# Kernel optimization log

Hardware: AMD Instinct MI355X
Metric: run time of the kernel (lower is better)

Reference implementation:

```python
import jax, jax.numpy as jnp
import numpy as np
from jax import lax

K = 3
PAD = 1
STRIDE = 1
DIL = 1
BN_EPS = 1e-5


def bilinear_gather(x, py, px):
    """Zero-padded bilinear sampling. x:[B,C,Hin,Win]; py,px:[B,T,H,W] -> [B,C,T,H,W]."""
    B, C, Hin, Win = x.shape
    xf = x.reshape(B, C, Hin * Win)
    y0 = jnp.floor(py)
    x0 = jnp.floor(px)
    wy1 = py - y0
    wx1 = px - x0
    wy0 = 1.0 - wy1
    wx0 = 1.0 - wx1

    def corner(yc, xc, w):
        valid = (yc >= 0) & (yc <= Hin - 1) & (xc >= 0) & (xc <= Win - 1)
        yi = jnp.clip(yc, 0, Hin - 1).astype(jnp.int32)
        xi = jnp.clip(xc, 0, Win - 1).astype(jnp.int32)
        idx = (yi * Win + xi).reshape(B, -1)  # [B, T*H*W]
        vals = jax.vmap(lambda xb, ib: xb[:, ib])(xf, idx)  # [B, C, T*H*W]
        vals = vals.reshape(B, C, *py.shape[1:])
        return vals * (w * valid.astype(x.dtype))[:, None]

    return (corner(y0, x0, wy0 * wx0) + corner(y0, x0 + 1.0, wy0 * wx1)
            + corner(y0 + 1.0, x0, wy1 * wx0) + corner(y0 + 1.0, x0 + 1.0, wy1 * wx1))


def setup_inputs() -> dict:
    key = jax.random.key(0)
    ks = jax.random.split(key, 6)
    B, C, H, W, O = 8, 128, 80, 80, 128
    x = jax.random.normal(ks[0], (B, C, H, W), dtype=jnp.float32)
    # offset/mask conv (zero-init in the module; small random here so sampling is exercised)
    w_off = jax.random.normal(ks[1], (3 * K * K, C, K, K), dtype=jnp.float32) * 0.05
    b_off = jax.random.normal(ks[2], (3 * K * K,), dtype=jnp.float32) * 0.01
    # main DCN weight: uniform(-std, std), std = 1/sqrt(C*K*K)
    std = 1.0 / float(np.sqrt(C * K * K))
    w_dcn = jax.random.uniform(ks[3], (O, C, K, K), dtype=jnp.float32, minval=-std, maxval=std)
    b_dcn = jax.random.normal(ks[4], (O,), dtype=jnp.float32) * 0.01
    gamma = jnp.ones((O,), dtype=jnp.float32)
    beta = jnp.zeros((O,), dtype=jnp.float32)
    return {"x": x, "w_dcn": w_dcn, "b_dcn": b_dcn, "w_off": w_off, "b_off": b_off,
            "gamma": gamma, "beta": beta}


def reference(x, w_dcn, b_dcn, w_off, b_off, gamma, beta):
    B, C, H, W = x.shape
    O = w_dcn.shape[0]
    # offset/mask conv (k=3, s=1, p=1) -> [B, 27, H, W]
    om = lax.conv_general_dilated(x, w_off, (STRIDE, STRIDE), [(PAD, PAD), (PAD, PAD)],
                                  dimension_numbers=("NCHW", "OIHW", "NCHW"))
    om = om + b_off[None, :, None, None]
    o1, o2, m = jnp.split(om, 3, axis=1)  # each [B, 9, H, W]
    mask = jax.nn.sigmoid(m)
    # torch: offset = cat(o1, o2); torchvision reads channel 2t as dy_t, 2t+1 as dx_t
    off = jnp.concatenate([o1, o2], axis=1).reshape(B, K * K, 2, H, W)
    dy, dx = off[:, :, 0], off[:, :, 1]  # [B, 9, H, W]
    ky, kx = jnp.meshgrid(jnp.arange(K), jnp.arange(K), indexing="ij")
    ky = ky.reshape(-1)
    kx = kx.reshape(-1)  # [9]
    base_y = (jnp.arange(H)[None, :, None] * STRIDE - PAD + ky[:, None, None] * DIL).astype(x.dtype)  # [9,H,1]
    base_x = (jnp.arange(W)[None, None, :] * STRIDE - PAD + kx[:, None, None] * DIL).astype(x.dtype)  # [9,1,W]
    py = dy + base_y[None]  # [B, 9, H, W]
    px = dx + base_x[None]
    sampled = bilinear_gather(x, py, px)  # [B, C, 9, H, W]
    sampled = sampled * mask[:, None]  # modulated (dg=1 broadcasts over C)
    wk = w_dcn.reshape(O, C, K * K)
    out = jnp.einsum("bckhw,ock->bohw", sampled, wk) + b_dcn[None, :, None, None]
    # BatchNorm (training-mode batch stats, biased variance) + SiLU
    mu = out.mean(axis=(0, 2, 3), keepdims=True)
    var = out.var(axis=(0, 2, 3), keepdims=True)
    y = (out - mu) * lax.rsqrt(var + BN_EPS) * gamma[None, :, None, None] + beta[None, :, None, None]
    return y * jax.nn.sigmoid(y)
```

## Files before the change

### kernel.cpp

```cpp
#include <hip/hip_runtime.h>
#include <hip/hip_bf16.h>
#include <hip/hip_fp16.h>

constexpr int B = 8, C = 128, H = 80, W = 80, O = 128;
constexpr int HW = H * W;
constexpr int NPIX = B * HW;
constexpr int KC = C * 9;
constexpr int DPX = 64;
constexpr int NBLK = NPIX / DPX;

typedef _Float16 h8 __attribute__((ext_vector_type(8)));
typedef _Float16 h2 __attribute__((ext_vector_type(2)));
typedef float f32x4 __attribute__((ext_vector_type(4)));

__device__ inline h8 as_h8(uint4 v) { h8 r; __builtin_memcpy(&r, &v, 16); return r; }
__device__ inline h2 u2h(uint u) { h2 r; __builtin_memcpy(&r, &u, 4); return r; }
__device__ inline uint h2u(h2 h) { uint r; __builtin_memcpy(&r, &h, 4); return r; }
__device__ inline uint pkh(float a, float b) {
  h2 h = { (_Float16)a, (_Float16)b };
  return h2u(h);
}
__device__ inline int swz16(int row, int byte) {
  return (row * 256 + (byte ^ ((row & 7) << 4))) >> 1;
}

__global__ __launch_bounds__(256) void k_xt(const float* __restrict__ x,
                                            _Float16* __restrict__ xt) {
  __shared__ uint tile32[64 * 64];
  const int t = threadIdx.x;
  const int p0 = blockIdx.x * 64;
  const int b = p0 / HW, hw0 = p0 - b * HW;
  const int w = t >> 6, l = t & 63;
#pragma unroll
  for (int j = 0; j < 16; ++j) {
    int c0 = (j * 4 + w) * 2;
    float f0 = x[((size_t)(b * C + c0)) * HW + hw0 + l];
    float f1 = x[((size_t)(b * C + c0 + 1)) * HW + hw0 + l];
    int byte = l * 256 + ((c0 * 2) ^ ((l & 7) << 4));
    tile32[byte >> 2] = pkh(f0, f1);
  }
  __syncthreads();
  _Float16* dst = xt + (size_t)(b * HW + hw0) * C;
#pragma unroll
  for (int it = 0; it < 4; ++it) {
    int g = w * 4096 + it * 1024 + l * 16;
    int row = g >> 8, inner = g & 255;
    uint4 v = *(const uint4*)((const char*)tile32 + row * 256 + (inner ^ ((row & 7) << 4)));
    *(uint4*)(dst + (g >> 1)) = v;
  }
}

__global__ __launch_bounds__(256) void k_wt2(const float* __restrict__ w_dcn,
                                             const float* __restrict__ w_off,
                                             _Float16* __restrict__ wt,
                                             _Float16* __restrict__ wof,
                                             _Float16* __restrict__ zrow) {
  int i = blockIdx.x * 256 + threadIdx.x;
  if (i < O * KC) {
    int c = i & 127, k = (i >> 7) % 9, o = i / KC;
    wt[i] = (_Float16)w_dcn[(size_t)o * KC + c * 9 + k];
  }
  if (i < 32 * KC) {
    int c = i & 127, k = (i >> 7) % 9, o = i / KC;
    wof[i] = (o < 27) ? (_Float16)w_off[((size_t)o * C + c) * 9 + k] : (_Float16)0.f;
  }
  if (i < 128) zrow[i] = (_Float16)0.f;
}

__global__ __launch_bounds__(256, 6) void k_offc4(
    const _Float16* __restrict__ xt, const _Float16* __restrict__ wof,
    const _Float16* __restrict__ zrow, const float* __restrict__ b_off,
    float* __restrict__ om) {
  const int t = threadIdx.x;
  const int bid = (blockIdx.x & 7) * 200 + (blockIdx.x >> 3);
  const int b = bid / 200, hw0 = (bid - b * 200) * 32;
  const int lane = t & 63, wv = t >> 6, rl = lane & 15, gh = lane >> 4;
  const int mi = wv & 1, nt = wv >> 1;
  const int px = hw0 + nt * 16 + rl;
  const int hp = px / W, wp = px - hp * W;
  const _Float16* xb = xt + (size_t)b * HW * C;
  f32x4 acc = {0.f, 0.f, 0.f, 0.f};
#pragma unroll
  for (int k = 0; k < 9; ++k) {
    int ky = k / 3, kx = k - ky * 3;
    int y = hp + ky - 1, xx = wp + kx - 1;
    bool ok = ((unsigned)y < (unsigned)H) && ((unsigned)xx < (unsigned)W);
    const _Float16* rowp = ok ? (xb + (size_t)(y * W + xx) * C) : zrow;
    const _Float16* aP = wof + (size_t)(mi * 16 + rl) * KC + k * 128 + gh * 8;
#pragma unroll
    for (int kk = 0; kk < 4; ++kk) {
      h8 av = *(const h8*)(aP + kk * 32);
      h8 bv = *(const h8*)(rowp + kk * 32 + gh * 8);
      acc = __builtin_amdgcn_mfma_f32_16x16x32_f16(av, bv, acc, 0, 0, 0);
    }
  }
  float* ob = om + (size_t)b * 27 * HW + hw0 + nt * 16 + rl;
#pragma unroll
  for (int r = 0; r < 4; ++r) {
    int oc = mi * 16 + gh * 4 + r;
    if (oc < 27) ob[(size_t)oc * HW] = acc[r] + b_off[oc];
  }
}

__global__ __launch_bounds__(256, 3) void k_dcn4(
    const _Float16* __restrict__ xt, const float* __restrict__ om,
    const _Float16* __restrict__ wt, float* __restrict__ outr,
    float* __restrict__ part2) {
  __shared__ float s_w[DPX][9][4];
  __shared__ int s_i[DPX][9][4];
  __shared__ __align__(16) ushort s_buf[2][DPX * 128];
  const int t = threadIdx.x;
  const int bid = (blockIdx.x & 7) * 100 + (blockIdx.x >> 3);
  const int b = bid / 100, hw0 = (bid - b * 100) * DPX;

  for (int idx = t; idx < DPX * 9; idx += 256) {
    int px = idx / 9, k = idx - (idx / 9) * 9;
    int hw = hw0 + px, h = hw / W, w = hw - (hw / W) * W;
    int ky = k / 3, kx = k - ky * 3;
    const float* omp = om + (size_t)b * 27 * HW + hw;
    float dy = omp[(size_t)(2 * k) * HW];
    float dx = omp[(size_t)(2 * k + 1) * HW];
    float mk = 1.0f / (1.0f + __expf(-omp[(size_t)(18 + k) * HW]));
    float py = dy + (float)(h - 1 + ky);
    float pxf = dx + (float)(w - 1 + kx);
    float y0f = floorf(py), x0f = floorf(pxf);
    float wy1 = py - y0f, wx1 = pxf - x0f;
    float wy0 = 1.0f - wy1, wx0 = 1.0f - wx1;
    int y0 = (int)y0f, x0 = (int)x0f;
    int y1 = y0 + 1, x1 = x0 + 1;
    bool vy0 = (y0 >= 0) && (y0 < H);
    bool vy1 = (y1 >= 0) && (y1 < H);
    bool vx0 = (x0 >= 0) && (x0 < W);
    bool vx1 = (x1 >= 0) && (x1 < W);
    int cy0 = min(max(y0, 0), H - 1), cy1 = min(max(y1, 0), H - 1);
    int cx0 = min(max(x0, 0), W - 1), cx1 = min(max(x1, 0), W - 1);
    s_w[px][k][0] = (vy0 && vx0) ? wy0 * wx0 * mk : 0.0f;
    s_w[px][k][1] = (vy0 && vx1) ? wy0 * wx1 * mk : 0.0f;
    s_w[px][k][2] = (vy1 && vx0) ? wy1 * wx0 * mk : 0.0f;
    s_w[px][k][3] = (vy1 && vx1) ? wy1 * wx1 * mk : 0.0f;
    s_i[px][k][0] = cy0 * W + cx0;
    s_i[px][k][1] = cy0 * W + cx1;
    s_i[px][k][2] = cy1 * W + cx0;
    s_i[px][k][3] = cy1 * W + cx1;
  }
  __syncthreads();

  const int sp = t >> 2, sq = t & 3;
  const _Float16* xbq = xt + (size_t)b * HW * C + sq * 32;
  const int lane = t & 63, wv = t >> 6, rl = lane & 15, gh = lane >> 4;
  const _Float16* wbase = wt + (size_t)(wv * 32 + rl) * KC + gh * 8;

  uint4 gA0, gA1, gA2, gA3, gB0, gB1, gB2, gB3;
  uint4 gC0, gC1, gC2, gC3, gD0, gD1, gD2, gD3;
  uint4 wA0, wA1, wA2, wA3, wB0, wB1, wB2, wB3;
  float cw0, cw1, cw2, cw3;

#define GL4(o0, o1, o2, o3, P)                                            \
  asm volatile("global_load_dwordx4 %0, %4, off\n\t"                      \
               "global_load_dwordx4 %1, %4, off offset:16\n\t"            \
               "global_load_dwordx4 %2, %4, off offset:32\n\t"            \
               "global_load_dwordx4 %3, %4, off offset:48"                \
               : "=&v"(o0), "=&v"(o1), "=&v"(o2), "=&v"(o3) : "v"(P))
#define WL4(o0, o1, o2, o3, P)                                            \
  asm volatile("global_load_dwordx4 %0, %4, off\n\t"                      \
               "global_load_dwordx4 %1, %4, off offset:64\n\t"            \
               "global_load_dwordx4 %2, %4, off offset:128\n\t"           \
               "global_load_dwordx4 %3, %4, off offset:192"               \
               : "=&v"(o0), "=&v"(o1), "=&v"(o2), "=&v"(o3) : "v"(P))

  auto GLOAD = [&](int k) {
    int4 ii = *(const int4*)&s_i[sp][k][0];
    float4 wf = *(const float4*)&s_w[sp][k][0];
    cw0 = wf.x; cw1 = wf.y; cw2 = wf.z; cw3 = wf.w;
    GL4(gA0, gA1, gA2, gA3, xbq + (size_t)ii.x * C);
    GL4(gB0, gB1, gB2, gB3, xbq + (size_t)ii.y * C);
    GL4(gC0, gC1, gC2, gC3, xbq + (size_t)ii.z * C);
    GL4(gD0, gD1, gD2, gD3, xbq + (size_t)ii.w * C);
  };
  auto WLOAD = [&](int k) {
    const _Float16* a0 = wbase + k * 128;
    WL4(wA0, wA1, wA2, wA3, a0);
    WL4(wB0, wB1, wB2, wB3, a0 + 16 * KC);
  };

  auto SWRITE = [&](ushort* buf) {
    uint qa[16] = {gA0.x, gA0.y, gA0.z, gA0.w, gA1.x, gA1.y, gA1.z, gA1.w,
                   gA2.x, gA2.y, gA2.z, gA2.w, gA3.x, gA3.y, gA3.z, gA3.w};
    uint qb[16] = {gB0.x, gB0.y, gB0.z, gB0.w, gB1.x, gB1.y, gB1.z, gB1.w,
                   gB2.x, gB2.y, gB2.z, gB2.w, gB3.x, gB3.y, gB3.z, gB3.w};
    uint qc[16] = {gC0.x, gC0.y, gC0.z, gC0.w, gC1.x, gC1.y, gC1.z, gC1.w,
                   gC2.x, gC2.y, gC2.z, gC2.w, gC3.x, gC3.y, gC3.z, gC3.w};
    uint qd[16] = {gD0.x, gD0.y, gD0.z, gD0.w, gD1.x, gD1.y, gD1.z, gD1.w,
                   gD2.x, gD2.y, gD2.z, gD2.w, gD3.x, gD3.y, gD3.z, gD3.w};
    h2 W0 = {(_Float16)cw0, (_Float16)cw0};
    h2 W1 = {(_Float16)cw1, (_Float16)cw1};
    h2 W2 = {(_Float16)cw2, (_Float16)cw2};
    h2 W3 = {(_Float16)cw3, (_Float16)cw3};
    uint r[16];
#pragma unroll
    for (int d = 0; d < 16; ++d) {
      h2 o = u2h(qa[d]) * W0 + u2h(qb[d]) * W1 + u2h(qc[d]) * W2 + u2h(qd[d]) * W3;
      r[d] = h2u(o);
    }
#pragma unroll
    for (int e = 0; e < 4; ++e)
      *(uint4*)(buf + swz16(sp, sq * 64 + e * 16)) =
          make_uint4(r[4 * e], r[4 * e + 1], r[4 * e + 2], r[4 * e + 3]);
  };

  f32x4 acc[2][4];
#pragma unroll
  for (int m = 0; m < 2; ++m)
#pragma unroll
    for (int nt = 0; nt < 4; ++nt) acc[m][nt] = {0.f, 0.f, 0.f, 0.f};

  auto COMP = [&](const ushort* buf) {
    h8 av0, av1, bv;
#define KSTEP(WA, WB, KB)                                                  \
  av0 = as_h8(WA); av1 = as_h8(WB);                                        \
  _Pragma("unroll")                                                        \
  for (int nt = 0; nt < 4; ++nt) {                                         \
    bv = *(const h8*)(buf + swz16(nt * 16 + rl, KB + gh * 16));            \
    acc[0][nt] = __builtin_amdgcn_mfma_f32_16x16x32_f16(av0, bv, acc[0][nt], 0, 0, 0); \
    acc[1][nt] = __builtin_amdgcn_mfma_f32_16x16x32_f16(av1, bv, acc[1][nt], 0, 0, 0); \
  }
    KSTEP(wA0, wB0, 0)
    KSTEP(wA1, wB1, 64)
    KSTEP(wA2, wB2, 128)
    KSTEP(wA3, wB3, 192)
#undef KSTEP
  };

  GLOAD(0); WLOAD(0);
  asm volatile("s_waitcnt vmcnt(8)" ::: "memory");
  __builtin_amdgcn_sched_barrier(0);
  SWRITE(s_buf[0]);
  __syncthreads();

  for (int k = 0; k < 9; ++k) {
    if (k < 8) GLOAD(k + 1);
    if (k < 8) asm volatile("s_waitcnt vmcnt(16)" ::: "memory");
    else       asm volatile("s_waitcnt vmcnt(0)" ::: "memory");
    __builtin_amdgcn_sched_barrier(0);
    COMP(s_buf[k & 1]);
    if (k < 8) {
      WLOAD(k + 1);
      asm volatile("s_waitcnt vmcnt(8)" ::: "memory");
      __builtin_amdgcn_sched_barrier(0);
      SWRITE(s_buf[(k + 1) & 1]);
      __syncthreads();
    }
  }
#undef GL4
#undef WL4

  float* outb = outr + (size_t)b * O * HW + hw0 + rl;
  const int nb = blockIdx.x;
#pragma unroll
  for (int mi = 0; mi < 2; ++mi)
#pragma unroll
    for (int r = 0; r < 4; ++r) {
      int o = wv * 32 + mi * 16 + gh * 4 + r;
      float s = 0.f, s2 = 0.f;
#pragma unroll
      for (int nt = 0; nt < 4; ++nt) {
        float v = acc[mi][nt][r];
        outb[(size_t)o * HW + nt * 16] = v;
        s += v;
        s2 = fmaf(v, v, s2);
      }
#pragma unroll
      for (int m = 1; m < 16; m <<= 1) {
        s += __shfl_xor(s, m);
        s2 += __shfl_xor(s2, m);
      }
      if (rl == 0) {
        part2[(size_t)(2 * o) * NBLK + nb] = s;
        part2[(size_t)(2 * o + 1) * NBLK + nb] = s2;
      }
    }
}

__global__ __launch_bounds__(256) void k_bnred(const float* __restrict__ part2,
                                               float* __restrict__ stats) {
  const int j = blockIdx.x;
  float s = 0.f;
  for (int i = threadIdx.x; i < NBLK; i += 256) s += part2[(size_t)j * NBLK + i];
#pragma unroll
  for (int off = 32; off > 0; off >>= 1) s += __shfl_down(s, off);
  __shared__ float rs[4];
  int wid = threadIdx.x >> 6, lane = threadIdx.x & 63;
  if (lane == 0) rs[wid] = s;
  __syncthreads();
  if (threadIdx.x == 0) stats[j] = rs[0] + rs[1] + rs[2] + rs[3];
}

__global__ __launch_bounds__(256) void k_bnapply2(
    float* __restrict__ outr, const float* __restrict__ stats,
    const float* __restrict__ gamma, const float* __restrict__ beta) {
  const int n4 = B * O * HW / 4;
  for (int i = blockIdx.x * blockDim.x + threadIdx.x; i < n4;
       i += gridDim.x * blockDim.x) {
    int o = (i / (HW / 4)) % O;
    float S = stats[2 * o], S2 = stats[2 * o + 1];
    const float inv = 1.0f / (float)(B * HW);
    float mu = S * inv;
    float rstd = rsqrtf(fmaf(S2, inv, -mu * mu) + 1e-5f);
    float a = rstd * gamma[o];
    float bb = fmaf(-mu, a, beta[o]);
    float4 v = ((const float4*)outr)[i];
    float y0 = fmaf(v.x, a, bb);
    float y1 = fmaf(v.y, a, bb);
    float y2 = fmaf(v.z, a, bb);
    float y3 = fmaf(v.w, a, bb);
    v.x = y0 / (1.0f + __expf(-y0));
    v.y = y1 / (1.0f + __expf(-y1));
    v.z = y2 / (1.0f + __expf(-y2));
    v.w = y3 / (1.0f + __expf(-y3));
    ((float4*)outr)[i] = v;
  }
}

extern "C" void kernel_launch(void* const* d_in, const int* in_sizes, int n_in,
                              void* d_out, int out_size, void* d_ws, size_t ws_size,
                              hipStream_t stream) {
  const float* x = (const float*)d_in[0];
  const float* w_dcn = (const float*)d_in[1];
  const float* w_off = (const float*)d_in[3];
  const float* b_off = (const float*)d_in[4];
  const float* gamma = (const float*)d_in[5];
  const float* beta = (const float*)d_in[6];
  float* out = (float*)d_out;
  float* om = (float*)d_ws;
  _Float16* xt = (_Float16*)(om + (size_t)B * 27 * HW);
  _Float16* wt = xt + (size_t)B * HW * C;
  _Float16* wof = wt + (size_t)O * KC;
  float* part2 = (float*)(wof + (size_t)32 * KC);
  float* stats = part2 + (size_t)256 * NBLK;
  _Float16* zrow = (_Float16*)(stats + 256);

  k_xt<<<NPIX / 64, 256, 0, stream>>>(x, xt);
  k_wt2<<<(O * KC + 255) / 256, 256, 0, stream>>>(w_dcn, w_off, wt, wof, zrow);
  k_offc4<<<NPIX / 32, 256, 0, stream>>>(xt, wof, zrow, b_off, om);
  k_dcn4<<<NPIX / DPX, 256, 0, stream>>>(xt, om, wt, out, part2);
  k_bnred<<<256, 256, 0, stream>>>(part2, stats);
  k_bnapply2<<<2048, 256, 0, stream>>>(out, stats, gamma, beta);
}
```

Baseline: 230.5 us.

## Gather bilinear samples directly into MFMA registers, dropping LDS staging

The deformable-conv main kernel no longer stages interpolated samples through a double-buffered LDS tile with block barriers. Each wave now gathers and interpolates its own 16 pixels straight into MFMA B-operand registers and covers all 128 output channels per wave, loading weights directly from global memory (L2-cached). BN partial sums are combined across waves in shared memory before one store per block. This removes LDS writes, reads and syncs, but every wave re-reads the full weight slice, uses more accumulator registers (occupancy hint lowered from 3 to 2), and the weight loads are no longer prefetched.

```diff
diff --git a/kernel.cpp b/kernel.cpp
--- a/kernel.cpp
+++ b/kernel.cpp
@@ -19,9 +19,6 @@
 __device__ inline uint pkh(float a, float b) {
   h2 h = { (_Float16)a, (_Float16)b };
   return h2u(h);
-}
-__device__ inline int swz16(int row, int byte) {
-  return (row * 256 + (byte ^ ((row & 7) << 4))) >> 1;
 }
 
 __global__ __launch_bounds__(256) void k_xt(const float* __restrict__ x,
@@ -102,13 +99,13 @@
   }
 }
 
-__global__ __launch_bounds__(256, 3) void k_dcn4(
+__global__ __launch_bounds__(256, 2) void k_dcn5(
     const _Float16* __restrict__ xt, const float* __restrict__ om,
     const _Float16* __restrict__ wt, float* __restrict__ outr,
     float* __restrict__ part2) {
   __shared__ float s_w[DPX][9][4];
   __shared__ int s_i[DPX][9][4];
-  __shared__ __align__(16) ushort s_buf[2][DPX * 128];
+  __shared__ float s_red[2][128][4];
   const int t = threadIdx.x;
   const int bid = (blockIdx.x & 7) * 100 + (blockIdx.x >> 3);
   const int b = bid / 100, hw0 = (bid - b * 100) * DPX;
@@ -145,140 +142,108 @@
   }
   __syncthreads();
 
-  const int sp = t >> 2, sq = t & 3;
-  const _Float16* xbq = xt + (size_t)b * HW * C + sq * 32;
   const int lane = t & 63, wv = t >> 6, rl = lane & 15, gh = lane >> 4;
-  const _Float16* wbase = wt + (size_t)(wv * 32 + rl) * KC + gh * 8;
-
-  uint4 gA0, gA1, gA2, gA3, gB0, gB1, gB2, gB3;
-  uint4 gC0, gC1, gC2, gC3, gD0, gD1, gD2, gD3;
-  uint4 wA0, wA1, wA2, wA3, wB0, wB1, wB2, wB3;
-  float cw0, cw1, cw2, cw3;
-
-#define GL4(o0, o1, o2, o3, P)                                            \
-  asm volatile("global_load_dwordx4 %0, %4, off\n\t"                      \
-               "global_load_dwordx4 %1, %4, off offset:16\n\t"            \
-               "global_load_dwordx4 %2, %4, off offset:32\n\t"            \
-               "global_load_dwordx4 %3, %4, off offset:48"                \
+  const int mypx = wv * 16 + rl;
+  const _Float16* xb = xt + (size_t)b * HW * C + gh * 8;
+
+  uint4 pa0, pa1, pa2, pa3, pb0, pb1, pb2, pb3;
+  uint4 pc0, pc1, pc2, pc3, pd0, pd1, pd2, pd3;
+  float4 wf;
+
+#define GLD4(o0, o1, o2, o3, P)                                           \
+  asm volatile("global_load_dwordx4 %0, %4, off\n\t"                     \
+               "global_load_dwordx4 %1, %4, off offset:64\n\t"           \
+               "global_load_dwordx4 %2, %4, off offset:128\n\t"          \
+               "global_load_dwordx4 %3, %4, off offset:192"              \
                : "=&v"(o0), "=&v"(o1), "=&v"(o2), "=&v"(o3) : "v"(P))
-#define WL4(o0, o1, o2, o3, P)                                            \
-  asm volatile("global_load_dwordx4 %0, %4, off\n\t"                      \
-               "global_load_dwordx4 %1, %4, off offset:64\n\t"            \
-               "global_load_dwordx4 %2, %4, off offset:128\n\t"           \
-               "global_load_dwordx4 %3, %4, off offset:192"               \
-               : "=&v"(o0), "=&v"(o1), "=&v"(o2), "=&v"(o3) : "v"(P))
-
-  auto GLOAD = [&](int k) {
-    int4 ii = *(const int4*)&s_i[sp][k][0];
-    float4 wf = *(const float4*)&s_w[sp][k][0];
-    cw0 = wf.x; cw1 = wf.y; cw2 = wf.z; cw3 = wf.w;
-    GL4(gA0, gA1, gA2, gA3, xbq + (size_t)ii.x * C);
-    GL4(gB0, gB1, gB2, gB3, xbq + (size_t)ii.y * C);
-    GL4(gC0, gC1, gC2, gC3, xbq + (size_t)ii.z * C);
-    GL4(gD0, gD1, gD2, gD3, xbq + (size_t)ii.w * C);
+
+  auto ISSUE = [&](int k) {
+    int4 ii = *(const int4*)&s_i[mypx][k][0];
+    wf = *(const float4*)&s_w[mypx][k][0];
+    GLD4(pa0, pa1, pa2, pa3, xb + (size_t)ii.x * C);
+    GLD4(pb0, pb1, pb2, pb3, xb + (size_t)ii.y * C);
+    GLD4(pc0, pc1, pc2, pc3, xb + (size_t)ii.z * C);
+    GLD4(pd0, pd1, pd2, pd3, xb + (size_t)ii.w * C);
   };
-  auto WLOAD = [&](int k) {
-    const _Float16* a0 = wbase + k * 128;
-    WL4(wA0, wA1, wA2, wA3, a0);
-    WL4(wB0, wB1, wB2, wB3, a0 + 16 * KC);
-  };
-
-  auto SWRITE = [&](ushort* buf) {
-    uint qa[16] = {gA0.x, gA0.y, gA0.z, gA0.w, gA1.x, gA1.y, gA1.z, gA1.w,
-                   gA2.x, gA2.y, gA2.z, gA2.w, gA3.x, gA3.y, gA3.z, gA3.w};
-    uint qb[16] = {gB0.x, gB0.y, gB0.z, gB0.w, gB1.x, gB1.y, gB1.z, gB1.w,
-                   gB2.x, gB2.y, gB2.z, gB2.w, gB3.x, gB3.y, gB3.z, gB3.w};
-    uint qc[16] = {gC0.x, gC0.y, gC0.z, gC0.w, gC1.x, gC1.y, gC1.z, gC1.w,
-                   gC2.x, gC2.y, gC2.z, gC2.w, gC3.x, gC3.y, gC3.z, gC3.w};
-    uint qd[16] = {gD0.x, gD0.y, gD0.z, gD0.w, gD1.x, gD1.y, gD1.z, gD1.w,
-                   gD2.x, gD2.y, gD2.z, gD2.w, gD3.x, gD3.y, gD3.z, gD3.w};
-    h2 W0 = {(_Float16)cw0, (_Float16)cw0};
-    h2 W1 = {(_Float16)cw1, (_Float16)cw1};
-    h2 W2 = {(_Float16)cw2, (_Float16)cw2};
-    h2 W3 = {(_Float16)cw3, (_Float16)cw3};
-    uint r[16];
-#pragma unroll
-    for (int d = 0; d < 16; ++d) {
-      h2 o = u2h(qa[d]) * W0 + u2h(qb[d]) * W1 + u2h(qc[d]) * W2 + u2h(qd[d]) * W3;
-      r[d] = h2u(o);
+
+  f32x4 acc[8];
+#pragma unroll
+  for (int m = 0; m < 8; ++m) acc[m] = {0.f, 0.f, 0.f, 0.f};
+
+  ISSUE(0);
+  __builtin_amdgcn_sched_barrier(0);
+
+  for (int k = 0; k < 9; ++k) {
+    h2 W0 = {(_Float16)wf.x, (_Float16)wf.x};
+    h2 W1 = {(_Float16)wf.y, (_Float16)wf.y};
+    h2 W2 = {(_Float16)wf.z, (_Float16)wf.z};
+    h2 W3 = {(_Float16)wf.w, (_Float16)wf.w};
+    uint4 bf0, bf1, bf2, bf3;
+
+    asm volatile("s_waitcnt vmcnt(8)" ::: "memory");
+    __builtin_amdgcn_sched_barrier(0);
+#define I1(DST, A, Bq)                                                    \
+  DST.x = h2u(u2h(A.x) * W0 + u2h(Bq.x) * W1);                            \
+  DST.y = h2u(u2h(A.y) * W0 + u2h(Bq.y) * W1);                            \
+  DST.z = h2u(u2h(A.z) * W0 + u2h(Bq.z) * W1);                            \
+  DST.w = h2u(u2h(A.w) * W0 + u2h(Bq.w) * W1);
+    I1(bf0, pa0, pb0) I1(bf1, pa1, pb1) I1(bf2, pa2, pb2) I1(bf3, pa3, pb3)
+#undef I1
+    asm volatile("s_waitcnt vmcnt(0)" ::: "memory");
+    __builtin_amdgcn_sched_barrier(0);
+#define I2(DST, Cq, D)                                                    \
+  DST.x = h2u(u2h(DST.x) + u2h(Cq.x) * W2 + u2h(D.x) * W3);               \
+  DST.y = h2u(u2h(DST.y) + u2h(Cq.y) * W2 + u2h(D.y) * W3);               \
+  DST.z = h2u(u2h(DST.z) + u2h(Cq.z) * W2 + u2h(D.z) * W3);               \
+  DST.w = h2u(u2h(DST.w) + u2h(Cq.w) * W2 + u2h(D.w) * W3);
+    I2(bf0, pc0, pd0) I2(bf1, pc1, pd1) I2(bf2, pc2, pd2) I2(bf3, pc3, pd3)
+#undef I2
+    __builtin_amdgcn_sched_barrier(0);
+
+    h8 b0 = as_h8(bf0), b1 = as_h8(bf1), b2 = as_h8(bf2), b3 = as_h8(bf3);
+    __builtin_amdgcn_s_setprio(1);
+#pragma unroll
+    for (int m = 0; m < 8; ++m) {
+      const _Float16* ap = wt + (size_t)(m * 16 + rl) * KC + k * 128 + gh * 8;
+      acc[m] = __builtin_amdgcn_mfma_f32_16x16x32_f16(*(const h8*)(ap), b0, acc[m], 0, 0, 0);
+      acc[m] = __builtin_amdgcn_mfma_f32_16x16x32_f16(*(const h8*)(ap + 32), b1, acc[m], 0, 0, 0);
+      acc[m] = __builtin_amdgcn_mfma_f32_16x16x32_f16(*(const h8*)(ap + 64), b2, acc[m], 0, 0, 0);
+      acc[m] = __builtin_amdgcn_mfma_f32_16x16x32_f16(*(const h8*)(ap + 96), b3, acc[m], 0, 0, 0);
     }
-#pragma unroll
-    for (int e = 0; e < 4; ++e)
-      *(uint4*)(buf + swz16(sp, sq * 64 + e * 16)) =
-          make_uint4(r[4 * e], r[4 * e + 1], r[4 * e + 2], r[4 * e + 3]);
-  };
-
-  f32x4 acc[2][4];
-#pragma unroll
-  for (int m = 0; m < 2; ++m)
-#pragma unroll
-    for (int nt = 0; nt < 4; ++nt) acc[m][nt] = {0.f, 0.f, 0.f, 0.f};
-
-  auto COMP = [&](const ushort* buf) {
-    h8 av0, av1, bv;
-#define KSTEP(WA, WB, KB)                                                  \
-  av0 = as_h8(WA); av1 = as_h8(WB);                                        \
-  _Pragma("unroll")                                                        \
-  for (int nt = 0; nt < 4; ++nt) {                                         \
-    bv = *(const h8*)(buf + swz16(nt * 16 + rl, KB + gh * 16));            \
-    acc[0][nt] = __builtin_amdgcn_mfma_f32_16x16x32_f16(av0, bv, acc[0][nt], 0, 0, 0); \
-    acc[1][nt] = __builtin_amdgcn_mfma_f32_16x16x32_f16(av1, bv, acc[1][nt], 0, 0, 0); \
-  }
-    KSTEP(wA0, wB0, 0)
-    KSTEP(wA1, wB1, 64)
-    KSTEP(wA2, wB2, 128)
-    KSTEP(wA3, wB3, 192)
-#undef KSTEP
-  };
-
-  GLOAD(0); WLOAD(0);
-  asm volatile("s_waitcnt vmcnt(8)" ::: "memory");
-  __builtin_amdgcn_sched_barrier(0);
-  SWRITE(s_buf[0]);
-  __syncthreads();
-
-  for (int k = 0; k < 9; ++k) {
-    if (k < 8) GLOAD(k + 1);
-    if (k < 8) asm volatile("s_waitcnt vmcnt(16)" ::: "memory");
-    else       asm volatile("s_waitcnt vmcnt(0)" ::: "memory");
+    __builtin_amdgcn_s_setprio(0);
     __builtin_amdgcn_sched_barrier(0);
-    COMP(s_buf[k & 1]);
     if (k < 8) {
-      WLOAD(k + 1);
-      asm volatile("s_waitcnt vmcnt(8)" ::: "memory");
+      ISSUE(k + 1);
       __builtin_amdgcn_sched_barrier(0);
-      SWRITE(s_buf[(k + 1) & 1]);
-      __syncthreads();
     }
   }
-#undef GL4
-#undef WL4
-
-  float* outb = outr + (size_t)b * O * HW + hw0 + rl;
-  const int nb = blockIdx.x;
-#pragma unroll
-  for (int mi = 0; mi < 2; ++mi)
+#undef GLD4
+
+  float* outb = outr + (size_t)b * O * HW + hw0 + wv * 16 + rl;
+#pragma unroll
+  for (int m = 0; m < 8; ++m)
 #pragma unroll
     for (int r = 0; r < 4; ++r) {
-      int o = wv * 32 + mi * 16 + gh * 4 + r;
-      float s = 0.f, s2 = 0.f;
-#pragma unroll
-      for (int nt = 0; nt < 4; ++nt) {
-        float v = acc[mi][nt][r];
-        outb[(size_t)o * HW + nt * 16] = v;
-        s += v;
-        s2 = fmaf(v, v, s2);
-      }
-#pragma unroll
-      for (int m = 1; m < 16; m <<= 1) {
-        s += __shfl_xor(s, m);
-        s2 += __shfl_xor(s2, m);
+      int o = m * 16 + gh * 4 + r;
+      float v = acc[m][r];
+      outb[(size_t)o * HW] = v;
+      float s = v, s2 = v * v;
+#pragma unroll
+      for (int mm = 1; mm < 16; mm <<= 1) {
+        s += __shfl_xor(s, mm);
+        s2 += __shfl_xor(s2, mm);
       }
       if (rl == 0) {
-        part2[(size_t)(2 * o) * NBLK + nb] = s;
-        part2[(size_t)(2 * o + 1) * NBLK + nb] = s2;
+        s_red[0][o][wv] = s;
+        s_red[1][o][wv] = s2;
       }
     }
+  __syncthreads();
+  if (t < 256) {
+    int o = t & 127, st = t >> 7;
+    float s = s_red[st][o][0] + s_red[st][o][1] + s_red[st][o][2] + s_red[st][o][3];
+    part2[(size_t)(2 * o + st) * NBLK + blockIdx.x] = s;
+  }
 }
 
 __global__ __launch_bounds__(256) void k_bnred(const float* __restrict__ part2,
@@ -342,7 +307,7 @@
   k_xt<<<NPIX / 64, 256, 0, stream>>>(x, xt);
   k_wt2<<<(O * KC + 255) / 256, 256, 0, stream>>>(w_dcn, w_off, wt, wof, zrow);
   k_offc4<<<NPIX / 32, 256, 0, stream>>>(xt, wof, zrow, b_off, om);
-  k_dcn4<<<NPIX / DPX, 256, 0, stream>>>(xt, om, wt, out, part2);
+  k_dcn5<<<NBLK, 256, 0, stream>>>(xt, om, wt, out, part2);
   k_bnred<<<256, 256, 0, stream>>>(part2, stats);
   k_bnapply2<<<2048, 256, 0, stream>>>(out, stats, gamma, beta);
 }
```

New measurement: 354.2 us. 53.7% more time.
